# Kernel tuning notes

Hardware: AMD Instinct MI355X
Metric: run time of the kernel (lower is better)

Reference implementation:

```python
import jax, jax.numpy as jnp
import numpy as np

N_SYM = 128
BATCH = 131072
LEVERAGE = 30.0


def setup_inputs() -> dict:
    key = jax.random.key(0)
    ks = jax.random.split(key, 8)
    fractions = jax.random.normal(ks[0], (N_SYM, BATCH), dtype=jnp.float32)
    # exec_samples are Bernoulli(0/1) execution indicators, kept as float
    exec_samples = jnp.round(jax.random.uniform(ks[1], (N_SYM, BATCH), dtype=jnp.float32))
    pos_sizes = jax.random.normal(ks[2], (N_SYM, BATCH), dtype=jnp.float32)
    # margin rates strictly positive
    margin_rates = jax.random.uniform(ks[3], (N_SYM, BATCH), dtype=jnp.float32) * 0.9 + 0.1
    unused_margin = jax.random.uniform(ks[4], (BATCH,), dtype=jnp.float32) * 1000.0
    # per-symbol volume constraints: min == step (typical broker config), max >> min
    msm_step = jax.random.uniform(ks[5], (N_SYM,), dtype=jnp.float32) * 0.01 + 0.01
    msm_min = msm_step
    msm_max = msm_step * 1000.0
    return {
        "fractions": fractions,
        "exec_samples": exec_samples,
        "pos_sizes": pos_sizes,
        "margin_rates": margin_rates,
        "unused_margin": unused_margin,
        "msm_min": msm_min,
        "msm_step": msm_step,
        "msm_max": msm_max,
    }


def reference(fractions, exec_samples, pos_sizes, margin_rates, unused_margin,
              msm_min, msm_step, msm_max):
    """JAX port of LowLevelInferenceEngine._compute_new_pos_sizes.

    Sequential recurrence over traded symbols (axis 0), carrying
    unused_margin [BATCH]. Returns (new_pos_sizes [N_SYM, BATCH],
    final unused_margin [BATCH]).
    """

    def step_fn(um, xs):
        frac, ex, pos, mr, mn, st, mx = xs
        unused_size = um * mr * LEVERAGE
        max_pos_size = jnp.abs(pos) + unused_size
        # torch.where(pos*frac > 0, unused_size, max_pos_size).minimum(0)
        adj = jnp.minimum(jnp.where(pos * frac > 0, unused_size, max_pos_size), 0.0)
        new_pos_size = frac * (max_pos_size - adj)
        abs_nps = jnp.abs(new_pos_size)
        sgn = jnp.sign(new_pos_size)
        abs_nps = jnp.floor(abs_nps / st) * st
        abs_nps = jnp.where(abs_nps < mn, 0.0, abs_nps)
        abs_nps = jnp.minimum(abs_nps, mx)
        out = ex * (sgn * abs_nps) + (1.0 - ex) * pos
        um_new = (max_pos_size - abs_nps) / (mr * LEVERAGE)
        return um_new, out

    um_final, new_pos_sizes = jax.lax.scan(
        step_fn,
        unused_margin,
        (fractions, exec_samples, pos_sizes, margin_rates, msm_min, msm_step, msm_max),
    )
    return new_pos_sizes, um_final
```

## Files before the change

kernel.cpp:

```cpp
#include <hip/hip_runtime.h>
#include <math.h>

#define N_SYM 128
#define BATCH 131072
#define LEV   30.0f
#define RING  4
#define NGRP  (N_SYM / 4)

typedef float v4 __attribute__((ext_vector_type(4)));

__device__ __forceinline__ void gload16(const float* g, float* l)
{
    __builtin_amdgcn_global_load_lds(
        (const __attribute__((address_space(1))) void*)g,
        (__attribute__((address_space(3))) void*)l,
        16, 0, 0);
}

__device__ __forceinline__ float step1(float f, float e, float p, float m,
                                       float st, float mn, float mx,
                                       float* um)
{
    const float mrl = m * LEV;
    const float us  = *um * mrl;
    const float mps = fabsf(p) + us;
    const float adj = fminf((p * f > 0.0f) ? us : mps, 0.0f);
    const float nps = f * (mps - adj);

    float       a  = fabsf(nps);
    const float sg = copysignf(1.0f, nps);
    a = floorf(a / st) * st;
    a = (a < mn) ? 0.0f : a;
    a = fminf(a, mx);

    *um = (mps - a) / mrl;
    return e * (sg * a) + (1.0f - e) * p;
}

#define VMWAIT(N) asm volatile("s_waitcnt vmcnt(" #N ")" ::: "memory")

__global__ __launch_bounds__(64) void lle_wave_kernel(
    const float* __restrict__ frac,
    const float* __restrict__ exs,
    const float* __restrict__ pos,
    const float* __restrict__ mrate,
    const float* __restrict__ um0,
    const float* __restrict__ msm_min,
    const float* __restrict__ msm_step,
    const float* __restrict__ msm_max,
    float* __restrict__ out)
{
    __shared__ __align__(16) float lin[RING][4][4][64];
    __shared__ __align__(16) float lout[4][64];

    const int l       = threadIdx.x;
    const int colbase = blockIdx.x * 64;

    const float* srcs[4] = { frac, exs, pos, mrate };

    const size_t lrow = (size_t)(l >> 4);
    const size_t lcol = (size_t)colbase + 4 * (l & 15);

    auto issue = [&](int g) {
        const int slot = g & (RING - 1);
        const size_t row = (size_t)g * 4 + lrow;
#pragma unroll
        for (int A = 0; A < 4; ++A)
            gload16(srcs[A] + row * BATCH + lcol, &lin[slot][A][0][0]);
    };

    float um = um0[colbase + l];

    auto consume = [&](int g) {
        const int slot = g & (RING - 1);
#pragma unroll
        for (int j = 0; j < 4; ++j) {
            const int   s  = g * 4 + j;
            const float st = msm_step[s];
            const float mn = msm_min[s];
            const float mx = msm_max[s];
            const float f  = lin[slot][0][j][l];
            const float e  = lin[slot][1][j][l];
            const float pv = lin[slot][2][j][l];
            const float m  = lin[slot][3][j][l];
            lout[j][l] = step1(f, e, pv, m, st, mn, mx, &um);
        }
        const v4 ro = *(const v4*)&lout[l >> 4][4 * (l & 15)];
        __builtin_nontemporal_store(
            ro, (v4*)(out + ((size_t)g * 4 + lrow) * BATCH + lcol));
    };

    issue(0); issue(1); issue(2);

    issue(3); VMWAIT(12); consume(0);
    issue(4); VMWAIT(12); consume(1);
    issue(5); VMWAIT(12); consume(2);

    for (int g = 3; g <= NGRP - 4; ++g) {
        issue(g + 3);
        VMWAIT(15);
        consume(g);
    }

    VMWAIT(11); consume(NGRP - 3);
    VMWAIT(7);  consume(NGRP - 2);
    VMWAIT(3);  consume(NGRP - 1);

    __builtin_nontemporal_store(um, &out[(size_t)N_SYM * BATCH + colbase + l]);
}

extern "C" void kernel_launch(void* const* d_in, const int* in_sizes, int n_in,
                              void* d_out, int out_size, void* d_ws, size_t ws_size,
                              hipStream_t stream) {
    const float* frac     = (const float*)d_in[0];
    const float* exs      = (const float*)d_in[1];
    const float* pos      = (const float*)d_in[2];
    const float* mrate    = (const float*)d_in[3];
    const float* um0      = (const float*)d_in[4];
    const float* msm_min  = (const float*)d_in[5];
    const float* msm_step = (const float*)d_in[6];
    const float* msm_max  = (const float*)d_in[7];
    float* out = (float*)d_out;

    const int block = 64;
    const int grid  = BATCH / 64;

    hipLaunchKernelGGL(lle_wave_kernel, dim3(grid), dim3(block), 0, stream,
                       frac, exs, pos, mrate, um0, msm_min, msm_step, msm_max,
                       out);
}
```

Baseline: 285.1 us.

## Use 256-thread blocks with per-wave input streams staged through LDS

Replaces the single-wave kernel, which used global_load_lds direct-to-LDS loads, with a 256-thread block. Each wave loads one of the four input arrays into registers three phases ahead and writes them into a double-buffered LDS stage, then every thread runs the recurrence for its own column. Each wave now issues 1 KB contiguous row loads of a single array, and larger blocks should reduce per-block overhead. The cost is two block barriers per phase plus extra register staging and LDS write traffic, where the old scheme loaded directly into LDS.

After: 266.5 us. 6.5% less time.

```diff
diff --git a/kernel.cpp b/kernel.cpp
--- a/kernel.cpp
+++ b/kernel.cpp
@@ -4,18 +4,11 @@
 #define N_SYM 128
 #define BATCH 131072
 #define LEV   30.0f
-#define RING  4
-#define NGRP  (N_SYM / 4)
+#define G     4
+#define NPH   (N_SYM / G)
+#define CPB   256
 
 typedef float v4 __attribute__((ext_vector_type(4)));
-
-__device__ __forceinline__ void gload16(const float* g, float* l)
-{
-    __builtin_amdgcn_global_load_lds(
-        (const __attribute__((address_space(1))) void*)g,
-        (__attribute__((address_space(3))) void*)l,
-        16, 0, 0);
-}
 
 __device__ __forceinline__ float step1(float f, float e, float p, float m,
                                        float st, float mn, float mx,
@@ -38,8 +31,59 @@
 }
 
 #define VMWAIT(N) asm volatile("s_waitcnt vmcnt(" #N ")" ::: "memory")
+#define LGKM0()   asm volatile("s_waitcnt lgkmcnt(0)" ::: "memory")
+#define SCHED0()  __builtin_amdgcn_sched_barrier(0)
+#define BAR()     do { __builtin_amdgcn_s_barrier(); \
+                       asm volatile("" ::: "memory"); } while (0)
 
-__global__ __launch_bounds__(64) void lle_wave_kernel(
+#define LOADPH(PG, DST)                                                    \
+    do {                                                                   \
+        _Pragma("unroll")                                                  \
+        for (int _j = 0; _j < G; ++_j)                                     \
+            (DST)[_j] = *(const v4*)(mysrc +                               \
+                        (size_t)((PG) * G + _j) * BATCH + gcol);           \
+        SCHED0();                                                          \
+    } while (0)
+
+#define STAGE(SL, SRC)                                                     \
+    do {                                                                   \
+        _Pragma("unroll")                                                  \
+        for (int _j = 0; _j < G; ++_j)                                     \
+            *(v4*)&stg[SL][_j][wave][4 * lane] = (SRC)[_j];                \
+    } while (0)
+
+#define CONSUME(PG)                                                        \
+    do {                                                                   \
+        const int _sl = (PG) & 1;                                          \
+        _Pragma("unroll")                                                  \
+        for (int _j = 0; _j < G; ++_j) {                                   \
+            const int   _s  = (PG) * G + _j;                               \
+            const float _st = msm_step[_s];                                \
+            const float _mn = msm_min[_s];                                 \
+            const float _mx = msm_max[_s];                                 \
+            const float _f  = stg[_sl][_j][0][t];                          \
+            const float _e  = stg[_sl][_j][1][t];                          \
+            const float _pv = stg[_sl][_j][2][t];                          \
+            const float _m  = stg[_sl][_j][3][t];                          \
+            lout[_j][t] = step1(_f, _e, _pv, _m, _st, _mn, _mx, &um);      \
+        }                                                                  \
+    } while (0)
+
+#define GSTORE(PG)                                                         \
+    do {                                                                   \
+        const v4 _rv = *(const v4*)&lout[wave][4 * lane];                  \
+        __builtin_nontemporal_store(_rv,                                   \
+            (v4*)(out + (size_t)((PG) * G + wave) * BATCH + gcol));        \
+        SCHED0();                                                          \
+    } while (0)
+
+#define ROT3()                                                             \
+    do {                                                                   \
+        _Pragma("unroll")                                                  \
+        for (int _j = 0; _j < G; ++_j) { rA[_j] = rB[_j]; rB[_j] = rC[_j]; } \
+    } while (0)
+
+__global__ __launch_bounds__(256) void lle_xchg_kernel(
     const float* __restrict__ frac,
     const float* __restrict__ exs,
     const float* __restrict__ pos,
@@ -50,63 +94,71 @@
     const float* __restrict__ msm_max,
     float* __restrict__ out)
 {
-    __shared__ __align__(16) float lin[RING][4][4][64];
-    __shared__ __align__(16) float lout[4][64];
+    __shared__ __align__(16) float stg[2][G][4][CPB];
+    __shared__ __align__(16) float lout[G][CPB];
 
-    const int l       = threadIdx.x;
-    const int colbase = blockIdx.x * 64;
+    const int t    = threadIdx.x;
+    const int wave = t >> 6;
+    const int lane = t & 63;
+    const int C0   = blockIdx.x * CPB;
 
-    const float* srcs[4] = { frac, exs, pos, mrate };
+    const float* mysrc = (wave == 0) ? frac : (wave == 1) ? exs
+                       : (wave == 2) ? pos  : mrate;
+    const size_t gcol = (size_t)C0 + 4 * (size_t)lane;
 
-    const size_t lrow = (size_t)(l >> 4);
-    const size_t lcol = (size_t)colbase + 4 * (l & 15);
+    float um = um0[C0 + t];
 
-    auto issue = [&](int g) {
-        const int slot = g & (RING - 1);
-        const size_t row = (size_t)g * 4 + lrow;
-#pragma unroll
-        for (int A = 0; A < 4; ++A)
-            gload16(srcs[A] + row * BATCH + lcol, &lin[slot][A][0][0]);
-    };
+    v4 t0[G], rA[G], rB[G], rC[G];
 
-    float um = um0[colbase + l];
+    LOADPH(0, t0);
+    LOADPH(1, rA);
+    LOADPH(2, rB);
+    VMWAIT(8); SCHED0();
+    STAGE(0, t0);
+    LGKM0(); BAR();
 
-    auto consume = [&](int g) {
-        const int slot = g & (RING - 1);
-#pragma unroll
-        for (int j = 0; j < 4; ++j) {
-            const int   s  = g * 4 + j;
-            const float st = msm_step[s];
-            const float mn = msm_min[s];
-            const float mx = msm_max[s];
-            const float f  = lin[slot][0][j][l];
-            const float e  = lin[slot][1][j][l];
-            const float pv = lin[slot][2][j][l];
-            const float m  = lin[slot][3][j][l];
-            lout[j][l] = step1(f, e, pv, m, st, mn, mx, &um);
-        }
-        const v4 ro = *(const v4*)&lout[l >> 4][4 * (l & 15)];
-        __builtin_nontemporal_store(
-            ro, (v4*)(out + ((size_t)g * 4 + lrow) * BATCH + lcol));
-    };
+    CONSUME(0);
+    LGKM0(); BAR();
+    GSTORE(0);
+    VMWAIT(5); SCHED0();
+    STAGE(1, rA);
+    LOADPH(3, rC);
+    ROT3();
+    LGKM0(); BAR();
 
-    issue(0); issue(1); issue(2);
-
-    issue(3); VMWAIT(12); consume(0);
-    issue(4); VMWAIT(12); consume(1);
-    issue(5); VMWAIT(12); consume(2);
-
-    for (int g = 3; g <= NGRP - 4; ++g) {
-        issue(g + 3);
-        VMWAIT(15);
-        consume(g);
+#pragma unroll 1
+    for (int g = 1; g <= 28; ++g) {
+        CONSUME(g);
+        LGKM0(); BAR();
+        GSTORE(g);
+        VMWAIT(6); SCHED0();
+        STAGE((g + 1) & 1, rA);
+        LOADPH(g + 3, rC);
+        ROT3();
+        LGKM0(); BAR();
     }
 
-    VMWAIT(11); consume(NGRP - 3);
-    VMWAIT(7);  consume(NGRP - 2);
-    VMWAIT(3);  consume(NGRP - 1);
+    CONSUME(29);
+    LGKM0(); BAR();
+    GSTORE(29);
+    VMWAIT(6); SCHED0();
+    STAGE(0, rA);
+#pragma unroll
+    for (int j = 0; j < G; ++j) rA[j] = rB[j];
+    LGKM0(); BAR();
 
-    __builtin_nontemporal_store(um, &out[(size_t)N_SYM * BATCH + colbase + l]);
+    CONSUME(30);
+    LGKM0(); BAR();
+    GSTORE(30);
+    VMWAIT(2); SCHED0();
+    STAGE(1, rA);
+    LGKM0(); BAR();
+
+    CONSUME(31);
+    LGKM0(); BAR();
+    GSTORE(31);
+
+    __builtin_nontemporal_store(um, &out[(size_t)N_SYM * BATCH + C0 + t]);
 }
 
 extern "C" void kernel_launch(void* const* d_in, const int* in_sizes, int n_in,
@@ -122,10 +174,10 @@
     const float* msm_max  = (const float*)d_in[7];
     float* out = (float*)d_out;
 
-    const int block = 64;
-    const int grid  = BATCH / 64;
+    const int block = 256;
+    const int grid  = BATCH / CPB;
 
-    hipLaunchKernelGGL(lle_wave_kernel, dim3(grid), dim3(block), 0, stream,
+    hipLaunchKernelGGL(lle_xchg_kernel, dim3(grid), dim3(block), 0, stream,
                        frac, exs, pos, mrate, um0, msm_min, msm_step, msm_max,
                        out);
 }
```
